# Optimization experiments

Measured on AMD Instinct MI355X. Metric: run time of the kernel, lower is better.

## Reference

```python
import jax, jax.numpy as jnp
import numpy as np

N_NODES = 100000
NEG_SLOPE = 0.2


def gat_layer(x, src, dst, W, al, ar, b):
    # x: [N, F_in]; src/dst: [E]; W: [F_in, F_out]; al/ar/b: [F_out]
    h = x @ W                                  # [N, F_out]
    el = h @ al                                # [N] per-src attention term
    er = h @ ar                                # [N] per-dst attention term
    e = jax.nn.leaky_relu(el[src] + er[dst], NEG_SLOPE)   # [E]
    # edge softmax over incoming edges of each dst node (numerically stable)
    mx = jax.ops.segment_max(e, dst, num_segments=N_NODES)
    mx = jnp.where(jnp.isfinite(mx), mx, 0.0)  # zero-in-degree guard
    ex = jnp.exp(e - mx[dst])
    denom = jax.ops.segment_sum(ex, dst, num_segments=N_NODES)
    alpha = ex / jnp.maximum(denom[dst], 1e-9)             # [E]
    out = jax.ops.segment_sum(alpha[:, None] * h[src], dst, num_segments=N_NODES)
    return out + b


def setup_inputs() -> dict:
    key = jax.random.key(0)
    ks = jax.random.split(key, 11)
    N, E, F_in, F_h = N_NODES, 1600000, 128, 64
    x = jax.random.normal(ks[0], (N, F_in), dtype=jnp.float32)
    src = jax.random.randint(ks[1], (E,), 0, N, dtype=jnp.int32)
    dst = jax.random.randint(ks[2], (E,), 0, N, dtype=jnp.int32)
    s1 = 1.0 / np.sqrt(F_in)
    s2 = 1.0 / np.sqrt(F_h)
    W1 = jax.random.normal(ks[3], (F_in, F_h), dtype=jnp.float32) * s1
    al1 = jax.random.normal(ks[4], (F_h,), dtype=jnp.float32) * s2
    ar1 = jax.random.normal(ks[5], (F_h,), dtype=jnp.float32) * s2
    b1 = jnp.zeros((F_h,), dtype=jnp.float32)
    W2 = jax.random.normal(ks[6], (F_h, F_h), dtype=jnp.float32) * s2
    al2 = jax.random.normal(ks[7], (F_h,), dtype=jnp.float32) * s2
    ar2 = jax.random.normal(ks[8], (F_h,), dtype=jnp.float32) * s2
    b2 = jnp.zeros((F_h,), dtype=jnp.float32)
    return {"x": x, "src": src, "dst": dst, "W1": W1, "al1": al1, "ar1": ar1,
            "b1": b1, "W2": W2, "al2": al2, "ar2": ar2, "b2": b2}


def reference(x, src, dst, W1, al1, ar1, b1, W2, al2, ar2, b2):
    h = gat_layer(x, src, dst, W1, al1, ar1, b1)   # conv1, head squeezed
    h = jax.nn.relu(h)                              # dropout = identity (eval)
    h = gat_layer(h, src, dst, W2, al2, ar2, b2)   # conv2
    return h
```

## Files before the change

### kernel.cpp

```cpp
#include <hip/hip_runtime.h>
#include <hip/hip_fp16.h>

#define NNODES 100000
#define NEG_SLOPE 0.2f
#define NBK 49
#define BKSHIFT 11
#define BKMASK 2047
#define BCAP 35328
#define B1 4096
#define NSL (NBK * 8)

typedef _Float16 f16x8 __attribute__((ext_vector_type(8)));
typedef float f32x4 __attribute__((ext_vector_type(4)));


__global__ void k_init(int* __restrict__ gcur, int* __restrict__ offs, int N, int E) {
    int t = threadIdx.x;
    if (t < NBK) gcur[t] = t * BCAP;
    if (t == NBK) offs[N] = E;
}


__global__ __launch_bounds__(256) void k_bin(const int* __restrict__ src,
                                             const int* __restrict__ dst,
                                             int* __restrict__ gcur,
                                             int* __restrict__ be, int E) {
    __shared__ int lcnt[NBK], lbase[NBK], lcur[NBK];
    int t = threadIdx.x;
    int base = blockIdx.x * B1;
    if (t < NBK) lcnt[t] = 0;
    __syncthreads();
    int dreg[16];
#pragma unroll
    for (int j = 0; j < 16; ++j) {
        int e = base + j * 256 + t;
        dreg[j] = (e < E) ? dst[e] : -1;
        if (e < E) atomicAdd(&lcnt[dreg[j] >> BKSHIFT], 1);
    }
    __syncthreads();
    if (t < NBK) { lbase[t] = atomicAdd(&gcur[t], lcnt[t]); lcur[t] = 0; }
    __syncthreads();
#pragma unroll
    for (int j = 0; j < 16; ++j) {
        int e = base + j * 256 + t;
        if (e < E) {
            int d = dreg[j];
            int bk = d >> BKSHIFT;
            int p = lbase[bk] + atomicAdd(&lcur[bk], 1);
            be[p] = (src[e] << BKSHIFT) | (d & BKMASK);
        }
    }
}


__global__ __launch_bounds__(256) void k_offs(const int* __restrict__ be,
                                              const int* __restrict__ gcur,
                                              int* __restrict__ offs, int N) {
    __shared__ int cnt[2048];
    __shared__ int sb[2][256];
    __shared__ int rbeg;
    int B = blockIdx.x, t = threadIdx.x;
    int mycnt = gcur[B] - B * BCAP;
    int ebase = B * BCAP;

    for (int i = t; i < 2048; i += 256) cnt[i] = 0;
    if (t == 0) rbeg = 0;
    __syncthreads();
    for (int i = t; i < mycnt; i += 256) atomicAdd(&cnt[be[ebase + i] & BKMASK], 1);
    if (t < 64) {
        int v = (t < B) ? gcur[t] - t * BCAP : 0;
#pragma unroll
        for (int o = 32; o; o >>= 1) v += __shfl_xor(v, o);
        if (t == 0) rbeg = v;
    }
    __syncthreads();

    int loc[8], s = 0;
#pragma unroll
    for (int i = 0; i < 8; ++i) { loc[i] = s; s += cnt[8 * t + i]; }
    sb[0][t] = s;
    __syncthreads();
    int pi = 0;
    for (int d = 1; d < 256; d <<= 1) {
        int po = pi ^ 1;
        sb[po][t] = sb[pi][t] + (t >= d ? sb[pi][t - d] : 0);
        pi = po;
        __syncthreads();
    }
    int bas = rbeg + sb[pi][t] - s;

    int node0 = (B << BKSHIFT) + 8 * t;
#pragma unroll
    for (int i = 0; i < 8; ++i) {
        int node = node0 + i;
        if (node < N) offs[node] = bas + loc[i];
    }
}


__global__ __launch_bounds__(256, 4) void k_gemm1sc(
    const float* __restrict__ x, const float* __restrict__ W,
    const float* __restrict__ al, const float* __restrict__ ar,
    __half* __restrict__ h, float* __restrict__ el, float* __restrict__ er,
    int N, const int* __restrict__ gcur, const int* __restrict__ be,
    const int* __restrict__ offs, int* __restrict__ csr, int E) {

    __shared__ float4 SMEM[2048];
    int t = threadIdx.x;

    if ((int)blockIdx.x < NSL) {
        int* cur = (int*)SMEM;
        int b = blockIdx.x;
        int B = b >> 3, sl = b & 7;
        int mycnt = gcur[B] - B * BCAP;
        int ebase = B * BCAP;
        int node = (B << BKSHIFT) + sl * 256 + t;
        cur[t] = (node < N) ? offs[node] : 0;
        __syncthreads();
        for (int i = t; i < mycnt; i += 256) {
            int v = be[ebase + i];
            int loc = v & BKMASK;
            if ((loc >> 8) == sl) {
                int p = atomicAdd(&cur[loc & 255], 1);
                csr[p] = v >> BKSHIFT;
            }
        }
        return;
    }

    char* A  = (char*)SMEM;
    char* Bw = (char*)SMEM + 16384;
    int row0 = ((int)blockIdx.x - NSL) * 64;

    for (int i = t; i < 2048; i += 256) {
        int r = i >> 5, c4 = i & 31;
        int rr = row0 + r; if (rr > N - 1) rr = N - 1;
        float4 v = *(const float4*)(x + (size_t)rr * 128 + c4 * 4);
        int byte = r * 256 + ((c4 * 8) ^ ((r & 7) << 4));
        *(__half2*)(A + byte)     = __floats2half2_rn(v.x, v.y);
        *(__half2*)(A + byte + 4) = __floats2half2_rn(v.z, v.w);
    }
    for (int i = t; i < 2048; i += 256) {
        int k = i >> 4, c4 = (i & 15) * 4;
        float4 v = *(const float4*)(W + k * 64 + c4);
        int kb = k * 2;
        *(__half*)(Bw + (c4 + 0) * 256 + (kb ^ (((c4 + 0) & 7) << 4))) = __float2half(v.x);
        *(__half*)(Bw + (c4 + 1) * 256 + (kb ^ (((c4 + 1) & 7) << 4))) = __float2half(v.y);
        *(__half*)(Bw + (c4 + 2) * 256 + (kb ^ (((c4 + 2) & 7) << 4))) = __float2half(v.z);
        *(__half*)(Bw + (c4 + 3) * 256 + (kb ^ (((c4 + 3) & 7) << 4))) = __float2half(v.w);
    }
    __syncthreads();

    int w = t >> 6, l = t & 63, g = l >> 4, c = l & 15;
    int swz = (c & 7) << 4;
    const char* Ar = A + (w * 16 + c) * 256;

    f32x4 acc[4];
#pragma unroll
    for (int t2 = 0; t2 < 4; ++t2) acc[t2] = (f32x4){0.f, 0.f, 0.f, 0.f};
#pragma unroll
    for (int kk = 0; kk < 4; ++kk) {
        int kb = kk * 64 + g * 16;
        f16x8 av = *(const f16x8*)(Ar + (kb ^ swz));
#pragma unroll
        for (int t2 = 0; t2 < 4; ++t2) {
            f16x8 bv = *(const f16x8*)(Bw + (t2 * 16 + c) * 256 + (kb ^ swz));
            acc[t2] = __builtin_amdgcn_mfma_f32_16x16x32_f16(av, bv, acc[t2], 0, 0, 0);
        }
    }

    float alv[4], arv[4];
#pragma unroll
    for (int t2 = 0; t2 < 4; ++t2) { alv[t2] = al[t2 * 16 + c]; arv[t2] = ar[t2 * 16 + c]; }
#pragma unroll
    for (int r = 0; r < 4; ++r) {
        float e1 = 0.f, e2 = 0.f;
#pragma unroll
        for (int t2 = 0; t2 < 4; ++t2) {
            e1 = fmaf(acc[t2][r], alv[t2], e1);
            e2 = fmaf(acc[t2][r], arv[t2], e2);
        }
#pragma unroll
        for (int o = 1; o < 16; o <<= 1) { e1 += __shfl_xor(e1, o); e2 += __shfl_xor(e2, o); }
        int row = row0 + w * 16 + 4 * g + r;
        if (row < N) {
            if (c == 0) { el[row] = e1; er[row] = e2; }
#pragma unroll
            for (int t2 = 0; t2 < 4; ++t2)
                h[(size_t)row * 64 + t2 * 16 + c] = __float2half(acc[t2][r]);
        }
    }
}


__global__ __launch_bounds__(256, 4) void k_gemm2(
    const __half* __restrict__ xin, const float* __restrict__ W,
    const float* __restrict__ al, const float* __restrict__ ar,
    __half* __restrict__ h, float* __restrict__ el, float* __restrict__ er, int N) {

    __shared__ float4 AlR[512];
    __shared__ float4 WtR[512];
    char* A = (char*)AlR;
    char* Bw = (char*)WtR;
    int tid = threadIdx.x;
    int row0 = blockIdx.x * 64;

    for (int i = tid; i < 512; i += 256) {
        int r = i >> 3, o = i & 7;
        int rr = row0 + r; if (rr > N - 1) rr = N - 1;
        float4 v = *(const float4*)(xin + (size_t)rr * 64 + o * 8);
        *(float4*)(A + r * 128 + ((o * 16) ^ ((r & 7) << 4))) = v;
    }
    for (int i = tid; i < 1024; i += 256) {
        int k = i >> 4, c4 = (i & 15) * 4;
        float4 v = *(const float4*)(W + k * 64 + c4);
        int kb = k * 2;
        *(__half*)(Bw + (c4 + 0) * 128 + (kb ^ (((c4 + 0) & 7) << 4))) = __float2half(v.x);
        *(__half*)(Bw + (c4 + 1) * 128 + (kb ^ (((c4 + 1) & 7) << 4))) = __float2half(v.y);
        *(__half*)(Bw + (c4 + 2) * 128 + (kb ^ (((c4 + 2) & 7) << 4))) = __float2half(v.z);
        *(__half*)(Bw + (c4 + 3) * 128 + (kb ^ (((c4 + 3) & 7) << 4))) = __float2half(v.w);
    }
    __syncthreads();

    int w = tid >> 6, l = tid & 63, g = l >> 4, c = l & 15;
    int swz = (c & 7) << 4;
    const char* Ar = A + (w * 16 + c) * 128;

    f32x4 acc[4];
#pragma unroll
    for (int t2 = 0; t2 < 4; ++t2) acc[t2] = (f32x4){0.f, 0.f, 0.f, 0.f};
#pragma unroll
    for (int kk = 0; kk < 2; ++kk) {
        int kb = kk * 64 + g * 16;
        f16x8 av = *(const f16x8*)(Ar + (kb ^ swz));
#pragma unroll
        for (int t2 = 0; t2 < 4; ++t2) {
            f16x8 bv = *(const f16x8*)(Bw + (t2 * 16 + c) * 128 + (kb ^ swz));
            acc[t2] = __builtin_amdgcn_mfma_f32_16x16x32_f16(av, bv, acc[t2], 0, 0, 0);
        }
    }

    float alv[4], arv[4];
#pragma unroll
    for (int t2 = 0; t2 < 4; ++t2) { alv[t2] = al[t2 * 16 + c]; arv[t2] = ar[t2 * 16 + c]; }
#pragma unroll
    for (int r = 0; r < 4; ++r) {
        float e1 = 0.f, e2 = 0.f;
#pragma unroll
        for (int t2 = 0; t2 < 4; ++t2) {
            e1 = fmaf(acc[t2][r], alv[t2], e1);
            e2 = fmaf(acc[t2][r], arv[t2], e2);
        }
#pragma unroll
        for (int o = 1; o < 16; o <<= 1) { e1 += __shfl_xor(e1, o); e2 += __shfl_xor(e2, o); }
        int row = row0 + w * 16 + 4 * g + r;
        if (row < N) {
            if (c == 0) { el[row] = e1; er[row] = e2; }
#pragma unroll
            for (int t2 = 0; t2 < 4; ++t2)
                h[(size_t)row * 64 + t2 * 16 + c] = __float2half(acc[t2][r]);
        }
    }
}


__device__ inline float2 h2_to_f2(float bits) {
    return __half22float2(__builtin_bit_cast(__half2, bits));
}

template <bool OUT_HALF>
__global__ __launch_bounds__(256) void k_agg(const __half* __restrict__ h,
                                             const float* __restrict__ el,
                                             const float* __restrict__ er,
                                             const float* __restrict__ b,
                                             const int* __restrict__ offs,
                                             const int* __restrict__ csr_src,
                                             void* __restrict__ outp, int N, int relu) {
    int wave = threadIdx.x >> 6, lane = threadIdx.x & 63;
    int n = blockIdx.x * 4 + wave;
    if (n >= N) return;

    int beg = offs[n], end = offs[n + 1];
    int deg = end - beg;
    float ern = er[n];

    int g = lane >> 4;
    int fl = lane & 15;
    float4 accv = make_float4(0.f, 0.f, 0.f, 0.f);
    const size_t foff = 4 * (size_t)fl;

    if (deg <= 64) {
        int sidx = 0;
        float e = -1e30f;
        if (lane < deg) {
            sidx = csr_src[beg + lane];
            e = el[sidx] + ern;
            e = e > 0.f ? e : NEG_SLOPE * e;
        }
        float m = e;
#pragma unroll
        for (int o = 32; o; o >>= 1) m = fmaxf(m, __shfl_xor(m, o));
        float p = (lane < deg) ? __expf(e - m) : 0.f;
        float s = p;
#pragma unroll
        for (int o = 32; o; o >>= 1) s += __shfl_xor(s, o);
        float a = p * (1.f / fmaxf(s, 1e-9f));

        int iters = (deg + 3) >> 2;
        int pair = iters >> 1;
        int i = g;
        for (int t2 = 0; t2 < pair; ++t2, i += 8) {
            int s0 = __shfl(sidx, i), s1 = __shfl(sidx, i + 4);
            float w0 = __shfl(a, i), w1 = __shfl(a, i + 4);
            float2 r0 = *(const float2*)(h + (size_t)s0 * 64 + foff);
            float2 r1 = *(const float2*)(h + (size_t)s1 * 64 + foff);
            float2 f00 = h2_to_f2(r0.x), f01 = h2_to_f2(r0.y);
            float2 f10 = h2_to_f2(r1.x), f11 = h2_to_f2(r1.y);
            accv.x = fmaf(w0, f00.x, accv.x); accv.y = fmaf(w0, f00.y, accv.y);
            accv.z = fmaf(w0, f01.x, accv.z); accv.w = fmaf(w0, f01.y, accv.w);
            accv.x = fmaf(w1, f10.x, accv.x); accv.y = fmaf(w1, f10.y, accv.y);
            accv.z = fmaf(w1, f11.x, accv.z); accv.w = fmaf(w1, f11.y, accv.w);
        }
        if (iters & 1) {
            int s0 = __shfl(sidx, i);
            float w0 = __shfl(a, i);
            float2 r0 = *(const float2*)(h + (size_t)s0 * 64 + foff);
            float2 f00 = h2_to_f2(r0.x), f01 = h2_to_f2(r0.y);
            accv.x = fmaf(w0, f00.x, accv.x); accv.y = fmaf(w0, f00.y, accv.y);
            accv.z = fmaf(w0, f01.x, accv.z); accv.w = fmaf(w0, f01.y, accv.w);
        }
    } else {
        float m = -1e30f;
        for (int i = beg + lane; i < end; i += 64) {
            float e = el[csr_src[i]] + ern;
            e = e > 0.f ? e : NEG_SLOPE * e;
            m = fmaxf(m, e);
        }
#pragma unroll
        for (int o = 32; o; o >>= 1) m = fmaxf(m, __shfl_xor(m, o));
        float s = 0.f;
        for (int i = beg + lane; i < end; i += 64) {
            float e = el[csr_src[i]] + ern;
            e = e > 0.f ? e : NEG_SLOPE * e;
            s += __expf(e - m);
        }
#pragma unroll
        for (int o = 32; o; o >>= 1) s += __shfl_xor(s, o);
        float inv = 1.f / fmaxf(s, 1e-9f);

        for (int i = g; i < deg; i += 4) {
            int s0 = csr_src[beg + i];
            float e = el[s0] + ern;
            e = e > 0.f ? e : NEG_SLOPE * e;
            float w0 = __expf(e - m) * inv;
            float2 r0 = *(const float2*)(h + (size_t)s0 * 64 + foff);
            float2 f00 = h2_to_f2(r0.x), f01 = h2_to_f2(r0.y);
            accv.x = fmaf(w0, f00.x, accv.x); accv.y = fmaf(w0, f00.y, accv.y);
            accv.z = fmaf(w0, f01.x, accv.z); accv.w = fmaf(w0, f01.y, accv.w);
        }
    }

#pragma unroll
    for (int o = 16; o <= 32; o <<= 1) {
        accv.x += __shfl_xor(accv.x, o);
        accv.y += __shfl_xor(accv.y, o);
        accv.z += __shfl_xor(accv.z, o);
        accv.w += __shfl_xor(accv.w, o);
    }

    if (lane < 16) {
        float4 bv = *(const float4*)(b + foff);
        float ox = accv.x + bv.x, oy = accv.y + bv.y;
        float oz = accv.z + bv.z, ow = accv.w + bv.w;
        if (relu) {
            ox = fmaxf(ox, 0.f); oy = fmaxf(oy, 0.f);
            oz = fmaxf(oz, 0.f); ow = fmaxf(ow, 0.f);
        }
        if (OUT_HALF) {
            __half* oh = (__half*)outp + (size_t)n * 64 + foff;
            *(__half2*)(oh)     = __floats2half2_rn(ox, oy);
            *(__half2*)(oh + 2) = __floats2half2_rn(oz, ow);
        } else {
            *(float4*)((float*)outp + (size_t)n * 64 + foff) = make_float4(ox, oy, oz, ow);
        }
    }
}


extern "C" void kernel_launch(void* const* d_in, const int* in_sizes, int n_in,
                              void* d_out, int out_size, void* d_ws, size_t ws_size,
                              hipStream_t stream) {
    const float* x   = (const float*)d_in[0];
    const int*   src = (const int*)d_in[1];
    const int*   dst = (const int*)d_in[2];
    const float* W1  = (const float*)d_in[3];
    const float* al1 = (const float*)d_in[4];
    const float* ar1 = (const float*)d_in[5];
    const float* b1  = (const float*)d_in[6];
    const float* W2  = (const float*)d_in[7];
    const float* al2 = (const float*)d_in[8];
    const float* ar2 = (const float*)d_in[9];
    const float* b2  = (const float*)d_in[10];
    float* out = (float*)d_out;

    const int N = NNODES;
    const int E = in_sizes[1];

    __half* h    = (__half*)d_ws;
    __half* hmid = h + (size_t)N * 64;
    int*    be   = (int*)(hmid + (size_t)N * 64);
    int*    csr  = be + (size_t)NBK * BCAP;
    float*  el   = (float*)(csr + E);
    float*  er   = el + N;
    int*    offs = (int*)(er + N);
    int*    gcur = offs + N + 1;

    int nbBin = (E + B1 - 1) / B1;
    int nbG   = (N + 63) / 64;
    int nbR   = (N + 3) / 4;

    k_init<<<1, 64, 0, stream>>>(gcur, offs, N, E);
    k_bin<<<nbBin, 256, 0, stream>>>(src, dst, gcur, be, E);
    k_offs<<<NBK, 256, 0, stream>>>(be, gcur, offs, N);
    k_gemm1sc<<<NSL + nbG, 256, 0, stream>>>(x, W1, al1, ar1, h, el, er, N,
                                             gcur, be, offs, csr, E);
    k_agg<true><<<nbR, 256, 0, stream>>>(h, el, er, b1, offs, csr, hmid, N, 1);
    k_gemm2<<<nbG, 256, 0, stream>>>(hmid, W2, al2, ar2, h, el, er, N);
    k_agg<false><<<nbR, 256, 0, stream>>>(h, el, er, b2, offs, csr, out, N, 0);
}
```

Measured before the change: 225.8 us.

## Overlap GEMM1 with edge binning, split scatter into own kernel, unroll gather by four

Moves the layer-1 GEMM into the edge-binning launch instead of the scatter launch, so binning and GEMM blocks run concurrently. The CSR scatter becomes a standalone kernel whose blocks are strided by bucket to spread work across CUs. The aggregation gather loop is unrolled from two to four neighbours per iteration to put more loads in flight. The risk is that the standalone scatter now runs alone, the fused kernel uses more shared memory per block, and the wider unroll raises register use.

```diff
diff --git a/kernel.cpp b/kernel.cpp
--- a/kernel.cpp
+++ b/kernel.cpp
@@ -8,7 +8,7 @@
 #define BKMASK 2047
 #define BCAP 35328
 #define B1 4096
-#define NSL (NBK * 8)
+#define SLSTRIDE 56
 
 typedef _Float16 f16x8 __attribute__((ext_vector_type(8)));
 typedef float f32x4 __attribute__((ext_vector_type(4)));
@@ -21,33 +21,105 @@
 }
 
 
-__global__ __launch_bounds__(256) void k_bin(const int* __restrict__ src,
-                                             const int* __restrict__ dst,
-                                             int* __restrict__ gcur,
-                                             int* __restrict__ be, int E) {
+__global__ __launch_bounds__(256, 4) void k_gemm1b(
+    const float* __restrict__ x, const float* __restrict__ W,
+    const float* __restrict__ al, const float* __restrict__ ar,
+    __half* __restrict__ h, float* __restrict__ el, float* __restrict__ er,
+    int N, int nbBin,
+    const int* __restrict__ src, const int* __restrict__ dst,
+    int* __restrict__ gcur, int* __restrict__ be, int E) {
+
+    __shared__ float4 SMEM[2048];
     __shared__ int lcnt[NBK], lbase[NBK], lcur[NBK];
     int t = threadIdx.x;
-    int base = blockIdx.x * B1;
-    if (t < NBK) lcnt[t] = 0;
-    __syncthreads();
-    int dreg[16];
-#pragma unroll
-    for (int j = 0; j < 16; ++j) {
-        int e = base + j * 256 + t;
-        dreg[j] = (e < E) ? dst[e] : -1;
-        if (e < E) atomicAdd(&lcnt[dreg[j] >> BKSHIFT], 1);
-    }
-    __syncthreads();
-    if (t < NBK) { lbase[t] = atomicAdd(&gcur[t], lcnt[t]); lcur[t] = 0; }
-    __syncthreads();
-#pragma unroll
-    for (int j = 0; j < 16; ++j) {
-        int e = base + j * 256 + t;
-        if (e < E) {
-            int d = dreg[j];
-            int bk = d >> BKSHIFT;
-            int p = lbase[bk] + atomicAdd(&lcur[bk], 1);
-            be[p] = (src[e] << BKSHIFT) | (d & BKMASK);
+
+    if ((int)blockIdx.x < nbBin) {
+        int base = (int)blockIdx.x * B1;
+        if (t < NBK) lcnt[t] = 0;
+        __syncthreads();
+        int dreg[16];
+#pragma unroll
+        for (int j = 0; j < 16; ++j) {
+            int e = base + j * 256 + t;
+            dreg[j] = (e < E) ? dst[e] : -1;
+            if (e < E) atomicAdd(&lcnt[dreg[j] >> BKSHIFT], 1);
+        }
+        __syncthreads();
+        if (t < NBK) { lbase[t] = atomicAdd(&gcur[t], lcnt[t]); lcur[t] = 0; }
+        __syncthreads();
+#pragma unroll
+        for (int j = 0; j < 16; ++j) {
+            int e = base + j * 256 + t;
+            if (e < E) {
+                int d = dreg[j];
+                int bk = d >> BKSHIFT;
+                int p = lbase[bk] + atomicAdd(&lcur[bk], 1);
+                be[p] = (src[e] << BKSHIFT) | (d & BKMASK);
+            }
+        }
+        return;
+    }
+
+    char* A  = (char*)SMEM;
+    char* Bw = (char*)SMEM + 16384;
+    int row0 = ((int)blockIdx.x - nbBin) * 64;
+
+    for (int i = t; i < 2048; i += 256) {
+        int r = i >> 5, c4 = i & 31;
+        int rr = row0 + r; if (rr > N - 1) rr = N - 1;
+        float4 v = *(const float4*)(x + (size_t)rr * 128 + c4 * 4);
+        int byte = r * 256 + ((c4 * 8) ^ ((r & 7) << 4));
+        *(__half2*)(A + byte)     = __floats2half2_rn(v.x, v.y);
+        *(__half2*)(A + byte + 4) = __floats2half2_rn(v.z, v.w);
+    }
+    for (int i = t; i < 2048; i += 256) {
+        int k = i >> 4, c4 = (i & 15) * 4;
+        float4 v = *(const float4*)(W + k * 64 + c4);
+        int kb = k * 2;
+        *(__half*)(Bw + (c4 + 0) * 256 + (kb ^ (((c4 + 0) & 7) << 4))) = __float2half(v.x);
+        *(__half*)(Bw + (c4 + 1) * 256 + (kb ^ (((c4 + 1) & 7) << 4))) = __float2half(v.y);
+        *(__half*)(Bw + (c4 + 2) * 256 + (kb ^ (((c4 + 2) & 7) << 4))) = __float2half(v.z);
+        *(__half*)(Bw + (c4 + 3) * 256 + (kb ^ (((c4 + 3) & 7) << 4))) = __float2half(v.w);
+    }
+    __syncthreads();
+
+    int w = t >> 6, l = t & 63, g = l >> 4, c = l & 15;
+    int swz = (c & 7) << 4;
+    const char* Ar = A + (w * 16 + c) * 256;
+
+    f32x4 acc[4];
+#pragma unroll
+    for (int t2 = 0; t2 < 4; ++t2) acc[t2] = (f32x4){0.f, 0.f, 0.f, 0.f};
+#pragma unroll
+    for (int kk = 0; kk < 4; ++kk) {
+        int kb = kk * 64 + g * 16;
+        f16x8 av = *(const f16x8*)(Ar + (kb ^ swz));
+#pragma unroll
+        for (int t2 = 0; t2 < 4; ++t2) {
+            f16x8 bv = *(const f16x8*)(Bw + (t2 * 16 + c) * 256 + (kb ^ swz));
+            acc[t2] = __builtin_amdgcn_mfma_f32_16x16x32_f16(av, bv, acc[t2], 0, 0, 0);
+        }
+    }
+
+    float alv[4], arv[4];
+#pragma unroll
+    for (int t2 = 0; t2 < 4; ++t2) { alv[t2] = al[t2 * 16 + c]; arv[t2] = ar[t2 * 16 + c]; }
+#pragma unroll
+    for (int r = 0; r < 4; ++r) {
+        float e1 = 0.f, e2 = 0.f;
+#pragma unroll
+        for (int t2 = 0; t2 < 4; ++t2) {
+            e1 = fmaf(acc[t2][r], alv[t2], e1);
+            e2 = fmaf(acc[t2][r], arv[t2], e2);
+        }
+#pragma unroll
+        for (int o = 1; o < 16; o <<= 1) { e1 += __shfl_xor(e1, o); e2 += __shfl_xor(e2, o); }
+        int row = row0 + w * 16 + 4 * g + r;
+        if (row < N) {
+            if (c == 0) { el[row] = e1; er[row] = e2; }
+#pragma unroll
+            for (int t2 = 0; t2 < 4; ++t2)
+                h[(size_t)row * 64 + t2 * 16 + c] = __float2half(acc[t2][r]);
         }
     }
 }
@@ -98,96 +170,27 @@
 }
 
 
-__global__ __launch_bounds__(256, 4) void k_gemm1sc(
-    const float* __restrict__ x, const float* __restrict__ W,
-    const float* __restrict__ al, const float* __restrict__ ar,
-    __half* __restrict__ h, float* __restrict__ el, float* __restrict__ er,
-    int N, const int* __restrict__ gcur, const int* __restrict__ be,
-    const int* __restrict__ offs, int* __restrict__ csr, int E) {
-
-    __shared__ float4 SMEM[2048];
+__global__ __launch_bounds__(256) void k_scat(const int* __restrict__ be,
+                                              const int* __restrict__ gcur,
+                                              const int* __restrict__ offs,
+                                              int* __restrict__ csr, int N) {
+    int b = blockIdx.x;
+    int B = b % SLSTRIDE, sl = b / SLSTRIDE;
+    if (B >= NBK) return;
+
+    __shared__ int cur[256];
     int t = threadIdx.x;
-
-    if ((int)blockIdx.x < NSL) {
-        int* cur = (int*)SMEM;
-        int b = blockIdx.x;
-        int B = b >> 3, sl = b & 7;
-        int mycnt = gcur[B] - B * BCAP;
-        int ebase = B * BCAP;
-        int node = (B << BKSHIFT) + sl * 256 + t;
-        cur[t] = (node < N) ? offs[node] : 0;
-        __syncthreads();
-        for (int i = t; i < mycnt; i += 256) {
-            int v = be[ebase + i];
-            int loc = v & BKMASK;
-            if ((loc >> 8) == sl) {
-                int p = atomicAdd(&cur[loc & 255], 1);
-                csr[p] = v >> BKSHIFT;
-            }
-        }
-        return;
-    }
-
-    char* A  = (char*)SMEM;
-    char* Bw = (char*)SMEM + 16384;
-    int row0 = ((int)blockIdx.x - NSL) * 64;
-
-    for (int i = t; i < 2048; i += 256) {
-        int r = i >> 5, c4 = i & 31;
-        int rr = row0 + r; if (rr > N - 1) rr = N - 1;
-        float4 v = *(const float4*)(x + (size_t)rr * 128 + c4 * 4);
-        int byte = r * 256 + ((c4 * 8) ^ ((r & 7) << 4));
-        *(__half2*)(A + byte)     = __floats2half2_rn(v.x, v.y);
-        *(__half2*)(A + byte + 4) = __floats2half2_rn(v.z, v.w);
-    }
-    for (int i = t; i < 2048; i += 256) {
-        int k = i >> 4, c4 = (i & 15) * 4;
-        float4 v = *(const float4*)(W + k * 64 + c4);
-        int kb = k * 2;
-        *(__half*)(Bw + (c4 + 0) * 256 + (kb ^ (((c4 + 0) & 7) << 4))) = __float2half(v.x);
-        *(__half*)(Bw + (c4 + 1) * 256 + (kb ^ (((c4 + 1) & 7) << 4))) = __float2half(v.y);
-        *(__half*)(Bw + (c4 + 2) * 256 + (kb ^ (((c4 + 2) & 7) << 4))) = __float2half(v.z);
-        *(__half*)(Bw + (c4 + 3) * 256 + (kb ^ (((c4 + 3) & 7) << 4))) = __float2half(v.w);
-    }
-    __syncthreads();
-
-    int w = t >> 6, l = t & 63, g = l >> 4, c = l & 15;
-    int swz = (c & 7) << 4;
-    const char* Ar = A + (w * 16 + c) * 256;
-
-    f32x4 acc[4];
-#pragma unroll
-    for (int t2 = 0; t2 < 4; ++t2) acc[t2] = (f32x4){0.f, 0.f, 0.f, 0.f};
-#pragma unroll
-    for (int kk = 0; kk < 4; ++kk) {
-        int kb = kk * 64 + g * 16;
-        f16x8 av = *(const f16x8*)(Ar + (kb ^ swz));
-#pragma unroll
-        for (int t2 = 0; t2 < 4; ++t2) {
-            f16x8 bv = *(const f16x8*)(Bw + (t2 * 16 + c) * 256 + (kb ^ swz));
-            acc[t2] = __builtin_amdgcn_mfma_f32_16x16x32_f16(av, bv, acc[t2], 0, 0, 0);
-        }
-    }
-
-    float alv[4], arv[4];
-#pragma unroll
-    for (int t2 = 0; t2 < 4; ++t2) { alv[t2] = al[t2 * 16 + c]; arv[t2] = ar[t2 * 16 + c]; }
-#pragma unroll
-    for (int r = 0; r < 4; ++r) {
-        float e1 = 0.f, e2 = 0.f;
-#pragma unroll
-        for (int t2 = 0; t2 < 4; ++t2) {
-            e1 = fmaf(acc[t2][r], alv[t2], e1);
-            e2 = fmaf(acc[t2][r], arv[t2], e2);
-        }
-#pragma unroll
-        for (int o = 1; o < 16; o <<= 1) { e1 += __shfl_xor(e1, o); e2 += __shfl_xor(e2, o); }
-        int row = row0 + w * 16 + 4 * g + r;
-        if (row < N) {
-            if (c == 0) { el[row] = e1; er[row] = e2; }
-#pragma unroll
-            for (int t2 = 0; t2 < 4; ++t2)
-                h[(size_t)row * 64 + t2 * 16 + c] = __float2half(acc[t2][r]);
+    int mycnt = gcur[B] - B * BCAP;
+    int ebase = B * BCAP;
+    int node = (B << BKSHIFT) + sl * 256 + t;
+    cur[t] = (node < N) ? offs[node] : 0;
+    __syncthreads();
+    for (int i = t; i < mycnt; i += 256) {
+        int v = be[ebase + i];
+        int loc = v & BKMASK;
+        if ((loc >> 8) == sl) {
+            int p = atomicAdd(&cur[loc & 255], 1);
+            csr[p] = v >> BKSHIFT;
         }
     }
 }
@@ -307,21 +310,32 @@
         float a = p * (1.f / fmaxf(s, 1e-9f));
 
         int iters = (deg + 3) >> 2;
-        int pair = iters >> 1;
+        int quad = iters >> 2;
         int i = g;
-        for (int t2 = 0; t2 < pair; ++t2, i += 8) {
-            int s0 = __shfl(sidx, i), s1 = __shfl(sidx, i + 4);
-            float w0 = __shfl(a, i), w1 = __shfl(a, i + 4);
+        for (int t4 = 0; t4 < quad; ++t4, i += 16) {
+            int s0 = __shfl(sidx, i),     s1 = __shfl(sidx, i + 4);
+            int s2 = __shfl(sidx, i + 8), s3 = __shfl(sidx, i + 12);
+            float w0 = __shfl(a, i),     w1 = __shfl(a, i + 4);
+            float w2 = __shfl(a, i + 8), w3 = __shfl(a, i + 12);
             float2 r0 = *(const float2*)(h + (size_t)s0 * 64 + foff);
             float2 r1 = *(const float2*)(h + (size_t)s1 * 64 + foff);
+            float2 r2 = *(const float2*)(h + (size_t)s2 * 64 + foff);
+            float2 r3 = *(const float2*)(h + (size_t)s3 * 64 + foff);
             float2 f00 = h2_to_f2(r0.x), f01 = h2_to_f2(r0.y);
             float2 f10 = h2_to_f2(r1.x), f11 = h2_to_f2(r1.y);
+            float2 f20 = h2_to_f2(r2.x), f21 = h2_to_f2(r2.y);
+            float2 f30 = h2_to_f2(r3.x), f31 = h2_to_f2(r3.y);
             accv.x = fmaf(w0, f00.x, accv.x); accv.y = fmaf(w0, f00.y, accv.y);
             accv.z = fmaf(w0, f01.x, accv.z); accv.w = fmaf(w0, f01.y, accv.w);
             accv.x = fmaf(w1, f10.x, accv.x); accv.y = fmaf(w1, f10.y, accv.y);
             accv.z = fmaf(w1, f11.x, accv.z); accv.w = fmaf(w1, f11.y, accv.w);
-        }
-        if (iters & 1) {
+            accv.x = fmaf(w2, f20.x, accv.x); accv.y = fmaf(w2, f20.y, accv.y);
+            accv.z = fmaf(w2, f21.x, accv.z); accv.w = fmaf(w2, f21.y, accv.w);
+            accv.x = fmaf(w3, f30.x, accv.x); accv.y = fmaf(w3, f30.y, accv.y);
+            accv.z = fmaf(w3, f31.x, accv.z); accv.w = fmaf(w3, f31.y, accv.w);
+        }
+        int rem = iters & 3;
+        for (int rr2 = 0; rr2 < rem; ++rr2, i += 4) {
             int s0 = __shfl(sidx, i);
             float w0 = __shfl(a, i);
             float2 r0 = *(const float2*)(h + (size_t)s0 * 64 + foff);
@@ -420,10 +434,10 @@
     int nbR   = (N + 3) / 4;
 
     k_init<<<1, 64, 0, stream>>>(gcur, offs, N, E);
-    k_bin<<<nbBin, 256, 0, stream>>>(src, dst, gcur, be, E);
+    k_gemm1b<<<nbBin + nbG, 256, 0, stream>>>(x, W1, al1, ar1, h, el, er, N,
+                                              nbBin, src, dst, gcur, be, E);
     k_offs<<<NBK, 256, 0, stream>>>(be, gcur, offs, N);
-    k_gemm1sc<<<NSL + nbG, 256, 0, stream>>>(x, W1, al1, ar1, h, el, er, N,
-                                             gcur, be, offs, csr, E);
+    k_scat<<<8 * SLSTRIDE, 256, 0, stream>>>(be, gcur, offs, csr, N);
     k_agg<true><<<nbR, 256, 0, stream>>>(h, el, er, b1, offs, csr, hmid, N, 1);
     k_gemm2<<<nbG, 256, 0, stream>>>(hmid, W2, al2, ar2, h, el, er, N);
     k_agg<false><<<nbR, 256, 0, stream>>>(h, el, er, b2, offs, csr, out, N, 0);
```

Result: faster. 211.1 us (-6.5%).
